# Kernel tuning notes

Hardware: AMD Instinct MI355X
Metric: run time of the kernel (lower is better)

Reference implementation:

```python
import jax, jax.numpy as jnp
import numpy as np

B, D_IN, C, P = 8192, 2048, 1000, 256


def setup_inputs() -> dict:
    key = jax.random.key(0)
    ks = jax.random.split(key, 6)
    return {
        "x": jax.random.normal(ks[0], (B, D_IN), dtype=jnp.float32),
        "Wm": jax.random.normal(ks[1], (C, D_IN), dtype=jnp.float32) * (1.0 / np.sqrt(D_IN)),
        "bm": jax.random.normal(ks[2], (C,), dtype=jnp.float32) * 0.01,
        "u": jax.random.normal(ks[3], (P, C), dtype=jnp.float32),
        "v": jax.random.normal(ks[4], (P, C), dtype=jnp.float32),
        "w": jax.random.normal(ks[5], (P, 1), dtype=jnp.float32),
    }


def reference(x, Wm, bm, u, v, w):
    # Backbone: Linear(D_IN -> C) producing per-instance logits (B, C)
    preds = jnp.einsum("bd,cd->bc", x, Wm) + bm
    # Gated attention, fully batched (replaces per-instance Python loop):
    # tanh(u @ pred) * sigmoid(v @ pred)  -> (B, P)
    gated = jnp.tanh(jnp.einsum("bc,pc->bp", preds, u)) * jax.nn.sigmoid(
        jnp.einsum("bc,pc->bp", preds, v)
    )
    scores = (gated @ w).ravel()          # (B,)
    attention = jax.nn.softmax(scores)    # softmax over instances
    total_pred = jnp.sum(preds * attention[:, None])
    return preds, total_pred
```

## Files before the change

kernel.cpp:

```cpp
#include <hip/hip_runtime.h>
#include <hip/hip_fp16.h>

typedef _Float16 half8 __attribute__((ext_vector_type(8)));
typedef float f32x4 __attribute__((ext_vector_type(4)));

#define B_   8192
#define DIN  2048
#define C_   1000
#define CP   1024
#define NP2  512

static const size_t OFF_WH  = 0;
static const size_t OFF_UVH = OFF_WH  + (size_t)CP * DIN * 2;
static const size_t OFF_PH  = OFF_UVH + (size_t)NP2 * CP * 2;
static const size_t OFF_SC  = OFF_PH  + (size_t)B_ * CP * 2;
static const size_t OFF_RS  = OFF_SC  + (size_t)B_ * 4;
static const size_t WS_NEED = OFF_RS  + (size_t)B_ * 4;

#define FENCE asm volatile("" ::: "memory")
#define BARRIER do { FENCE; __builtin_amdgcn_s_barrier(); FENCE; } while (0)
#define VMCNT(n) asm volatile("s_waitcnt vmcnt(" #n ")" ::: "memory")
#define PRIO1 __builtin_amdgcn_s_setprio(1)
#define PRIO0 __builtin_amdgcn_s_setprio(0)

__device__ __forceinline__ void gload16(const void* g, void* l) {
  __builtin_amdgcn_global_load_lds(
      (const __attribute__((address_space(1))) void*)g,
      (__attribute__((address_space(3))) void*)l, 16, 0, 0);
}

__global__ __launch_bounds__(256) void prep_kernel(
    const float* __restrict__ Wm,
    const float* __restrict__ u, const float* __restrict__ v,
    _Float16* __restrict__ wh, _Float16* __restrict__ uvh,
    float* __restrict__ scores, float* __restrict__ rowsum)
{
  const long NW  = (long)CP * DIN / 8;
  const long NUV = (long)NP2 * CP / 8;
  const long NZ  = 2 * (long)B_ / 8;
  const long T   = NW + NUV + NZ;
  for (long idx = (long)blockIdx.x * blockDim.x + threadIdx.x; idx < T;
       idx += (long)gridDim.x * blockDim.x) {
    if (idx < NW) {
      long e = idx * 8;
      int row = (int)(e >> 11);
      half8 h;
      if (row < C_) {
        float4 p0 = *(const float4*)(Wm + e);
        float4 p1 = *(const float4*)(Wm + e + 4);
        h[0] = (_Float16)p0.x; h[1] = (_Float16)p0.y; h[2] = (_Float16)p0.z; h[3] = (_Float16)p0.w;
        h[4] = (_Float16)p1.x; h[5] = (_Float16)p1.y; h[6] = (_Float16)p1.z; h[7] = (_Float16)p1.w;
      } else {
        h = (half8)(_Float16)0.f;
      }
      *(half8*)(wh + e) = h;
    } else if (idx < NW + NUV) {
      long e = (idx - NW) * 8;
      int j = (int)(e >> 10);
      int k = (int)(e & 1023);
      const float* src = (j & 1) ? v : u;
      int p = j >> 1;
      half8 h;
      #pragma unroll
      for (int t = 0; t < 8; ++t) {
        int kk = k + t;
        h[t] = (kk < C_) ? (_Float16)src[(size_t)p * C_ + kk] : (_Float16)0.f;
      }
      *(half8*)(uvh + e) = h;
    } else {
      long e = (idx - NW - NUV) * 8;
      float4 z = {0.f, 0.f, 0.f, 0.f};
      if (e < B_) {
        *(float4*)(scores + e) = z; *(float4*)(scores + e + 4) = z;
      } else {
        long r = e - B_;
        *(float4*)(rowsum + r) = z; *(float4*)(rowsum + r + 4) = z;
      }
    }
  }
}

__global__ __launch_bounds__(512, 2) void gemm1_kernel(
    const float* __restrict__ x, const _Float16* __restrict__ wh,
    const float* __restrict__ bmv, float* __restrict__ preds,
    _Float16* __restrict__ predsh, float* __restrict__ rowsum)
{
  __shared__ __align__(16) char LB[3 * 32768 + 3 * 8192];
  const int tid  = threadIdx.x;
  const int lane = tid & 63;
  const int w    = tid >> 6;
  const int wm   = w >> 1;
  const int wn   = w & 1;
  const int bm0  = blockIdx.x * 256;
  const int bn0  = blockIdx.y * 128;

  f32x4 acc[4][4] = {};

  const int trow = tid >> 3;
  const float* pAx = x + (size_t)(bm0 + trow) * DIN + (((tid & 7) ^ (trow & 7)) << 2);
  const int brow = tid >> 2;
  const _Float16* pBx = wh + (size_t)(bn0 + brow) * DIN + ((((tid & 3) ^ ((brow >> 1) & 3)) << 3));

  int aoff[4][2], boff[4];
  #pragma unroll
  for (int m = 0; m < 4; ++m) {
    int ra = wm * 64 + m * 16 + (lane & 15);
    int c0 = (lane >> 4) * 2;
    aoff[m][0] = ra * 128 + (((c0)     ^ (ra & 7)) << 4);
    aoff[m][1] = ra * 128 + (((c0 + 1) ^ (ra & 7)) << 4);
  }
  #pragma unroll
  for (int n = 0; n < 4; ++n) {
    int rb = wn * 64 + n * 16 + (lane & 15);
    boff[n] = rb * 64 + ((((lane >> 4)) ^ ((rb >> 1) & 3)) << 4);
  }

  half8 Aa[4], Ba[4], Ab[4], Bb[4];

  auto stage = [&](int c) {
    #pragma unroll
    for (int k = 0; k < 4; ++k)
      gload16(pAx + (size_t)k * 64 * DIN, LB + c * 32768 + k * 8192 + w * 1024);
    gload16(pBx, LB + 98304 + c * 8192 + w * 1024);
    pAx += 32; pBx += 32;
  };
  auto rdFrag = [&](int c, half8 (&A)[4], half8 (&Bf)[4]) {
    const char* ab = LB + c * 32768;
    const char* bb = LB + 98304 + c * 8192;
    #pragma unroll
    for (int m = 0; m < 4; ++m) {
      f32x4 lo = *(const f32x4*)(ab + aoff[m][0]);
      f32x4 hi = *(const f32x4*)(ab + aoff[m][1]);
      half8 h;
      h[0] = (_Float16)lo[0]; h[1] = (_Float16)lo[1];
      h[2] = (_Float16)lo[2]; h[3] = (_Float16)lo[3];
      h[4] = (_Float16)hi[0]; h[5] = (_Float16)hi[1];
      h[6] = (_Float16)hi[2]; h[7] = (_Float16)hi[3];
      A[m] = h;
    }
    #pragma unroll
    for (int n = 0; n < 4; ++n)
      Bf[n] = *(const half8*)(bb + boff[n]);
  };
  auto mfAll = [&](half8 (&A)[4], half8 (&Bf)[4]) {
    PRIO1;
    #pragma unroll
    for (int m = 0; m < 4; ++m)
      #pragma unroll
      for (int n = 0; n < 4; ++n)
        acc[m][n] = __builtin_amdgcn_mfma_f32_16x16x32_f16(A[m], Bf[n], acc[m][n], 0, 0, 0);
    PRIO0;
  };

  stage(0);
  stage(1);
  VMCNT(5);
  BARRIER;
  rdFrag(0, Aa, Ba);

  int c0 = 0;
  #pragma unroll 1
  for (int t = 0; t < 62; t += 2) {
    const int c1 = (c0 == 2) ? 0 : c0 + 1;
    const int c2 = (c1 == 2) ? 0 : c1 + 1;

    stage(c2);
    VMCNT(5);
    BARRIER;
    rdFrag(c1, Ab, Bb);
    mfAll(Aa, Ba);
    BARRIER;

    stage(c0);
    VMCNT(5);
    BARRIER;
    rdFrag(c2, Aa, Ba);
    mfAll(Ab, Bb);
    BARRIER;

    c0 = c2;
  }

  VMCNT(0);
  BARRIER;
  rdFrag(0, Ab, Bb);
  mfAll(Aa, Ba);
  mfAll(Ab, Bb);

  float rp[4][4] = {};
  #pragma unroll
  for (int m = 0; m < 4; ++m) {
    #pragma unroll
    for (int n = 0; n < 4; ++n) {
      f32x4 d = acc[m][n];
      int gc = bn0 + wn * 64 + n * 16 + (lane & 15);
      float bias = (gc < C_) ? bmv[gc] : 0.f;
      #pragma unroll
      for (int j = 0; j < 4; ++j) {
        int gr = bm0 + wm * 64 + m * 16 + (lane >> 4) * 4 + j;
        float val = d[j] + bias;
        predsh[(size_t)gr * CP + gc] = (_Float16)val;
        if (gc < C_) preds[(size_t)gr * C_ + gc] = val;
        rp[m][j] += val;
      }
    }
  }
  #pragma unroll
  for (int m = 0; m < 4; ++m) {
    #pragma unroll
    for (int j = 0; j < 4; ++j) {
      float s = rp[m][j];
      s += __shfl_xor(s, 1); s += __shfl_xor(s, 2);
      s += __shfl_xor(s, 4); s += __shfl_xor(s, 8);
      if ((lane & 15) == 0) {
        int gr = bm0 + wm * 64 + m * 16 + (lane >> 4) * 4 + j;
        atomicAdd(&rowsum[gr], s);
      }
    }
  }
}

__global__ __launch_bounds__(256) void gemm2_kernel(
    const _Float16* __restrict__ predsh, const _Float16* __restrict__ uvh,
    const float* __restrict__ wv, float* __restrict__ scores)
{
  __shared__ _Float16 sA[2][64 * 64];
  __shared__ _Float16 sB[2][128 * 64];
  const int tid  = threadIdx.x;
  const int lane = tid & 63;
  const int w    = tid >> 6;
  const int wm   = w >> 1, wn = w & 1;
  const int bm0  = blockIdx.x * 64;
  const int bn0  = blockIdx.y * 128;

  f32x4 acc[2][4] = {};

  const _Float16* srcA[2]; const _Float16* srcB[4];
  #pragma unroll
  for (int i = 0; i < 2; ++i) {
    int slot = i * 256 + tid;
    int row  = slot >> 3;
    int cb   = (slot & 7) << 4;
    int scb  = cb ^ ((row & 7) << 4);
    srcA[i] = predsh + (size_t)(bm0 + row) * CP + (scb >> 1);
  }
  #pragma unroll
  for (int i = 0; i < 4; ++i) {
    int slot = i * 256 + tid;
    int row  = slot >> 3;
    int cb   = (slot & 7) << 4;
    int scb  = cb ^ ((row & 7) << 4);
    srcB[i] = uvh + (size_t)(bn0 + row) * CP + (scb >> 1);
  }
  int aoff[2][2], boff[4][2];
  #pragma unroll
  for (int ks = 0; ks < 2; ++ks) {
    int kb = ks * 64 + (lane >> 4) * 16;
    #pragma unroll
    for (int mi = 0; mi < 2; ++mi) {
      int ra = wm * 32 + mi * 16 + (lane & 15);
      aoff[mi][ks] = ra * 128 + (kb ^ ((ra & 7) << 4));
    }
    #pragma unroll
    for (int ni = 0; ni < 4; ++ni) {
      int rb = wn * 64 + ni * 16 + (lane & 15);
      boff[ni][ks] = rb * 128 + (kb ^ ((rb & 7) << 4));
    }
  }

  auto stage = [&](int c) {
    #pragma unroll
    for (int i = 0; i < 2; ++i) {
      gload16(srcA[i], &sA[c][(i * 4 + w) * 512]);
      srcA[i] += 64;
    }
    #pragma unroll
    for (int i = 0; i < 4; ++i) {
      gload16(srcB[i], &sB[c][(i * 4 + w) * 512]);
      srcB[i] += 64;
    }
  };

  auto compute = [&](int c) {
    const char* bA = (const char*)&sA[c][0];
    const char* bB = (const char*)&sB[c][0];
    #pragma unroll
    for (int ks = 0; ks < 2; ++ks) {
      half8 a[2], b[4];
      #pragma unroll
      for (int mi = 0; mi < 2; ++mi) a[mi] = *(const half8*)(bA + aoff[mi][ks]);
      #pragma unroll
      for (int ni = 0; ni < 4; ++ni) b[ni] = *(const half8*)(bB + boff[ni][ks]);
      #pragma unroll
      for (int mi = 0; mi < 2; ++mi)
        #pragma unroll
        for (int ni = 0; ni < 4; ++ni)
          acc[mi][ni] = __builtin_amdgcn_mfma_f32_16x16x32_f16(a[mi], b[ni], acc[mi][ni], 0, 0, 0);
    }
  };

  const int NT = CP / 64;
  stage(0);
  #pragma unroll 1
  for (int kt = 0; kt < NT; kt += 2) {
    stage(1);
    asm volatile("s_waitcnt vmcnt(6)" ::: "memory");
    BARRIER;
    compute(0);
    BARRIER;
    if (kt + 2 < NT) {
      stage(0);
      asm volatile("s_waitcnt vmcnt(6)" ::: "memory");
    } else {
      asm volatile("s_waitcnt vmcnt(0)" ::: "memory");
    }
    BARRIER;
    compute(1);
    BARRIER;
  }

  float sp[2][4] = {};
  #pragma unroll
  for (int mi = 0; mi < 2; ++mi) {
    #pragma unroll
    for (int ni = 0; ni < 4; ++ni) {
      f32x4 d = acc[mi][ni];
      int gc = bn0 + wn * 64 + ni * 16 + (lane & 15);
      float wq = wv[gc >> 1];
      bool even = ((gc & 1) == 0);
      #pragma unroll
      for (int j = 0; j < 4; ++j) {
        float t  = d[j];
        float pr = __shfl_xor(t, 1);
        float th = 2.f / (1.f + __expf(-2.f * t)) - 1.f;
        float sg = 1.f / (1.f + __expf(-pr));
        sp[mi][j] += even ? (th * sg * wq) : 0.f;
      }
    }
  }
  #pragma unroll
  for (int mi = 0; mi < 2; ++mi) {
    #pragma unroll
    for (int j = 0; j < 4; ++j) {
      float s = sp[mi][j];
      s += __shfl_xor(s, 1); s += __shfl_xor(s, 2);
      s += __shfl_xor(s, 4); s += __shfl_xor(s, 8);
      if ((lane & 15) == 0) {
        int gr = bm0 + wm * 32 + mi * 16 + (lane >> 4) * 4 + j;
        atomicAdd(&scores[gr], s);
      }
    }
  }
}

__global__ __launch_bounds__(1024) void final_kernel(
    const float* __restrict__ scores, const float* __restrict__ rowsum,
    float* __restrict__ out)
{
  __shared__ float red[16], red2[16];
  const int t = threadIdx.x;
  const int lane = t & 63, wid = t >> 6;
  float s[8];
  float m = -3.4e38f;
  #pragma unroll
  for (int i = 0; i < 8; ++i) { s[i] = scores[t + i * 1024]; m = fmaxf(m, s[i]); }
  #pragma unroll
  for (int off = 1; off < 64; off <<= 1) m = fmaxf(m, __shfl_xor(m, off));
  if (lane == 0) red[wid] = m;
  __syncthreads();
  #pragma unroll
  for (int i = 0; i < 16; ++i) m = fmaxf(m, red[i]);
  __syncthreads();

  float se = 0.f, sr = 0.f;
  #pragma unroll
  for (int i = 0; i < 8; ++i) {
    float e = __expf(s[i] - m);
    se += e;
    sr += e * rowsum[t + i * 1024];
  }
  #pragma unroll
  for (int off = 1; off < 64; off <<= 1) { se += __shfl_xor(se, off); sr += __shfl_xor(sr, off); }
  if (lane == 0) { red[wid] = se; red2[wid] = sr; }
  __syncthreads();
  if (t == 0) {
    float tse = 0.f, tsr = 0.f;
    for (int i = 0; i < 16; ++i) { tse += red[i]; tsr += red2[i]; }
    out[0] = tsr / tse;
  }
}

extern "C" void kernel_launch(void* const* d_in, const int* in_sizes, int n_in,
                              void* d_out, int out_size, void* d_ws, size_t ws_size,
                              hipStream_t stream)
{
  const float* x   = (const float*)d_in[0];
  const float* Wm  = (const float*)d_in[1];
  const float* bmv = (const float*)d_in[2];
  const float* u   = (const float*)d_in[3];
  const float* v   = (const float*)d_in[4];
  const float* wv  = (const float*)d_in[5];
  float* out = (float*)d_out;

  if (ws_size < WS_NEED) return;

  char* ws = (char*)d_ws;
  _Float16* wh     = (_Float16*)(ws + OFF_WH);
  _Float16* uvh    = (_Float16*)(ws + OFF_UVH);
  _Float16* predsh = (_Float16*)(ws + OFF_PH);
  float*    scores = (float*)(ws + OFF_SC);
  float*    rowsum = (float*)(ws + OFF_RS);

  prep_kernel<<<1288, 256, 0, stream>>>(Wm, u, v, wh, uvh, scores, rowsum);
  gemm1_kernel<<<dim3(32, 8), 512, 0, stream>>>(x, wh, bmv, out, predsh, rowsum);
  gemm2_kernel<<<dim3(128, 4), 256, 0, stream>>>(predsh, uvh, wv, scores);
  final_kernel<<<1, 1024, 0, stream>>>(scores, rowsum, out + (size_t)B_ * C_);
}
```

Measured before the change: 93.59 us.

## Pre-convert x to fp16 and restructure gemm1 pipeline with 64-wide K tiles

```diff
diff --git a/kernel.cpp b/kernel.cpp
--- a/kernel.cpp
+++ b/kernel.cpp
@@ -10,7 +10,8 @@
 #define CP   1024
 #define NP2  512
 
-static const size_t OFF_WH  = 0;
+static const size_t OFF_XH  = 0;
+static const size_t OFF_WH  = OFF_XH  + (size_t)B_ * DIN * 2;
 static const size_t OFF_UVH = OFF_WH  + (size_t)CP * DIN * 2;
 static const size_t OFF_PH  = OFF_UVH + (size_t)NP2 * CP * 2;
 static const size_t OFF_SC  = OFF_PH  + (size_t)B_ * CP * 2;
@@ -20,6 +21,8 @@
 #define FENCE asm volatile("" ::: "memory")
 #define BARRIER do { FENCE; __builtin_amdgcn_s_barrier(); FENCE; } while (0)
 #define VMCNT(n) asm volatile("s_waitcnt vmcnt(" #n ")" ::: "memory")
+#define LGKM(n)  asm volatile("s_waitcnt lgkmcnt(" #n ")" ::: "memory")
+#define SCHED0   __builtin_amdgcn_sched_barrier(0)
 #define PRIO1 __builtin_amdgcn_s_setprio(1)
 #define PRIO0 __builtin_amdgcn_s_setprio(0)
 
@@ -30,19 +33,29 @@
 }
 
 __global__ __launch_bounds__(256) void prep_kernel(
-    const float* __restrict__ Wm,
+    const float* __restrict__ x, const float* __restrict__ Wm,
     const float* __restrict__ u, const float* __restrict__ v,
-    _Float16* __restrict__ wh, _Float16* __restrict__ uvh,
-    float* __restrict__ scores, float* __restrict__ rowsum)
+    _Float16* __restrict__ xh, _Float16* __restrict__ wh,
+    _Float16* __restrict__ uvh, float* __restrict__ scores,
+    float* __restrict__ rowsum)
 {
+  const long NX  = (long)B_ * DIN / 8;
   const long NW  = (long)CP * DIN / 8;
   const long NUV = (long)NP2 * CP / 8;
   const long NZ  = 2 * (long)B_ / 8;
-  const long T   = NW + NUV + NZ;
+  const long T   = NX + NW + NUV + NZ;
   for (long idx = (long)blockIdx.x * blockDim.x + threadIdx.x; idx < T;
        idx += (long)gridDim.x * blockDim.x) {
-    if (idx < NW) {
+    if (idx < NX) {
       long e = idx * 8;
+      float4 p0 = *(const float4*)(x + e);
+      float4 p1 = *(const float4*)(x + e + 4);
+      half8 h;
+      h[0] = (_Float16)p0.x; h[1] = (_Float16)p0.y; h[2] = (_Float16)p0.z; h[3] = (_Float16)p0.w;
+      h[4] = (_Float16)p1.x; h[5] = (_Float16)p1.y; h[6] = (_Float16)p1.z; h[7] = (_Float16)p1.w;
+      *(half8*)(xh + e) = h;
+    } else if (idx < NX + NW) {
+      long e = (idx - NX) * 8;
       int row = (int)(e >> 11);
       half8 h;
       if (row < C_) {
@@ -54,8 +67,8 @@
         h = (half8)(_Float16)0.f;
       }
       *(half8*)(wh + e) = h;
-    } else if (idx < NW + NUV) {
-      long e = (idx - NW) * 8;
+    } else if (idx < NX + NW + NUV) {
+      long e = (idx - NX - NW) * 8;
       int j = (int)(e >> 10);
       int k = (int)(e & 1023);
       const float* src = (j & 1) ? v : u;
@@ -68,7 +81,7 @@
       }
       *(half8*)(uvh + e) = h;
     } else {
-      long e = (idx - NW - NUV) * 8;
+      long e = (idx - NX - NW - NUV) * 8;
       float4 z = {0.f, 0.f, 0.f, 0.f};
       if (e < B_) {
         *(float4*)(scores + e) = z; *(float4*)(scores + e + 4) = z;
@@ -80,12 +93,13 @@
   }
 }
 
-__global__ __launch_bounds__(512, 2) void gemm1_kernel(
-    const float* __restrict__ x, const _Float16* __restrict__ wh,
+__global__ __launch_bounds__(512, 1) void gemm1_kernel(
+    const _Float16* __restrict__ xh, const _Float16* __restrict__ wh,
     const float* __restrict__ bmv, float* __restrict__ preds,
     _Float16* __restrict__ predsh, float* __restrict__ rowsum)
 {
-  __shared__ __align__(16) char LB[3 * 32768 + 3 * 8192];
+  __shared__ _Float16 lds[(3 * 32768 + 3 * 16384) / 2];
+  char* const LB = (char*)lds;
   const int tid  = threadIdx.x;
   const int lane = tid & 63;
   const int w    = tid >> 6;
@@ -97,95 +111,122 @@
   f32x4 acc[4][4] = {};
 
   const int trow = tid >> 3;
-  const float* pAx = x + (size_t)(bm0 + trow) * DIN + (((tid & 7) ^ (trow & 7)) << 2);
-  const int brow = tid >> 2;
-  const _Float16* pBx = wh + (size_t)(bn0 + brow) * DIN + ((((tid & 3) ^ ((brow >> 1) & 3)) << 3));
-
-  int aoff[4][2], boff[4];
-  #pragma unroll
-  for (int m = 0; m < 4; ++m) {
-    int ra = wm * 64 + m * 16 + (lane & 15);
-    int c0 = (lane >> 4) * 2;
-    aoff[m][0] = ra * 128 + (((c0)     ^ (ra & 7)) << 4);
-    aoff[m][1] = ra * 128 + (((c0 + 1) ^ (ra & 7)) << 4);
-  }
-  #pragma unroll
-  for (int n = 0; n < 4; ++n) {
-    int rb = wn * 64 + n * 16 + (lane & 15);
-    boff[n] = rb * 64 + ((((lane >> 4)) ^ ((rb >> 1) & 3)) << 4);
-  }
-
-  half8 Aa[4], Ba[4], Ab[4], Bb[4];
-
-  auto stage = [&](int c) {
-    #pragma unroll
-    for (int k = 0; k < 4; ++k)
-      gload16(pAx + (size_t)k * 64 * DIN, LB + c * 32768 + k * 8192 + w * 1024);
-    gload16(pBx, LB + 98304 + c * 8192 + w * 1024);
-    pAx += 32; pBx += 32;
-  };
-  auto rdFrag = [&](int c, half8 (&A)[4], half8 (&Bf)[4]) {
-    const char* ab = LB + c * 32768;
-    const char* bb = LB + 98304 + c * 8192;
-    #pragma unroll
-    for (int m = 0; m < 4; ++m) {
-      f32x4 lo = *(const f32x4*)(ab + aoff[m][0]);
-      f32x4 hi = *(const f32x4*)(ab + aoff[m][1]);
-      half8 h;
-      h[0] = (_Float16)lo[0]; h[1] = (_Float16)lo[1];
-      h[2] = (_Float16)lo[2]; h[3] = (_Float16)lo[3];
-      h[4] = (_Float16)hi[0]; h[5] = (_Float16)hi[1];
-      h[6] = (_Float16)hi[2]; h[7] = (_Float16)hi[3];
-      A[m] = h;
-    }
-    #pragma unroll
-    for (int n = 0; n < 4; ++n)
-      Bf[n] = *(const half8*)(bb + boff[n]);
-  };
-  auto mfAll = [&](half8 (&A)[4], half8 (&Bf)[4]) {
+  const int swzc = (((tid & 7) << 4) ^ ((trow & 7) << 4)) >> 1;
+  const _Float16* pA = xh + (size_t)(bm0 + trow) * DIN + swzc;
+  const _Float16* pB = wh + (size_t)(bn0 + trow) * DIN + swzc;
+
+  int aoff[4][2], boff[4][2];
+  #pragma unroll
+  for (int m = 0; m < 4; ++m)
+    #pragma unroll
+    for (int ks = 0; ks < 2; ++ks) {
+      int ra = wm * 64 + m * 16 + (lane & 15);
+      int kb = ks * 64 + (lane >> 4) * 16;
+      aoff[m][ks] = ra * 128 + (kb ^ ((ra & 7) << 4));
+    }
+  #pragma unroll
+  for (int n = 0; n < 4; ++n)
+    #pragma unroll
+    for (int ks = 0; ks < 2; ++ks) {
+      int rb = wn * 64 + n * 16 + (lane & 15);
+      int kb = ks * 64 + (lane >> 4) * 16;
+      boff[n][ks] = rb * 128 + (kb ^ ((rb & 7) << 4));
+    }
+
+  half8 A[4][2], Bf[4][2];
+
+  auto stageH1 = [&](int c) {
+    #pragma unroll
+    for (int k = 0; k < 3; ++k)
+      gload16(pA + (size_t)k * 64 * DIN, LB + c * 32768 + k * 8192 + w * 1024);
+  };
+  auto stageH2 = [&](int c) {
+    gload16(pA + (size_t)3 * 64 * DIN, LB + c * 32768 + 3 * 8192 + w * 1024);
+    #pragma unroll
+    for (int k = 0; k < 2; ++k)
+      gload16(pB + (size_t)k * 64 * DIN, LB + 98304 + c * 16384 + k * 8192 + w * 1024);
+    pA += 64; pB += 64;
+  };
+  auto rdA = [&](int c) {
+    const char* b = LB + c * 32768;
+    #pragma unroll
+    for (int m = 0; m < 4; ++m)
+      #pragma unroll
+      for (int ks = 0; ks < 2; ++ks)
+        A[m][ks] = *(const half8*)(b + aoff[m][ks]);
+  };
+  auto rdB01 = [&](int c) {
+    const char* b = LB + 98304 + c * 16384;
+    #pragma unroll
+    for (int n = 0; n < 2; ++n)
+      #pragma unroll
+      for (int ks = 0; ks < 2; ++ks)
+        Bf[n][ks] = *(const half8*)(b + boff[n][ks]);
+  };
+  auto rdB23 = [&](int c) {
+    const char* b = LB + 98304 + c * 16384;
+    #pragma unroll
+    for (int n = 2; n < 4; ++n)
+      #pragma unroll
+      for (int ks = 0; ks < 2; ++ks)
+        Bf[n][ks] = *(const half8*)(b + boff[n][ks]);
+  };
+  auto mfH = [&](int nlo) {
     PRIO1;
     #pragma unroll
     for (int m = 0; m < 4; ++m)
       #pragma unroll
-      for (int n = 0; n < 4; ++n)
-        acc[m][n] = __builtin_amdgcn_mfma_f32_16x16x32_f16(A[m], Bf[n], acc[m][n], 0, 0, 0);
+      for (int n = nlo; n < nlo + 2; ++n)
+        #pragma unroll
+        for (int ks = 0; ks < 2; ++ks)
+          acc[m][n] = __builtin_amdgcn_mfma_f32_16x16x32_f16(A[m][ks], Bf[n][ks], acc[m][n], 0, 0, 0);
     PRIO0;
   };
 
-  stage(0);
-  stage(1);
-  VMCNT(5);
+  stageH1(0); stageH2(0);
+  stageH1(1); stageH2(1);
+  VMCNT(6);
   BARRIER;
-  rdFrag(0, Aa, Ba);
 
   int c0 = 0;
   #pragma unroll 1
-  for (int t = 0; t < 62; t += 2) {
-    const int c1 = (c0 == 2) ? 0 : c0 + 1;
-    const int c2 = (c1 == 2) ? 0 : c1 + 1;
-
-    stage(c2);
-    VMCNT(5);
-    BARRIER;
-    rdFrag(c1, Ab, Bb);
-    mfAll(Aa, Ba);
-    BARRIER;
-
-    stage(c0);
-    VMCNT(5);
-    BARRIER;
-    rdFrag(c2, Aa, Ba);
-    mfAll(Ab, Bb);
-    BARRIER;
-
-    c0 = c2;
-  }
-
+  for (int t = 0; t < 30; ++t) {
+    const int c2 = (c0 >= 1) ? c0 - 1 : 2;
+
+    rdA(c0); rdB01(c0);
+    stageH1(c2);
+    LGKM(8);
+    BARRIER;
+    LGKM(0); SCHED0;
+    mfH(0);
+    BARRIER;
+
+    rdB23(c0);
+    stageH2(c2);
+    VMCNT(6);
+    BARRIER;
+    LGKM(0); SCHED0;
+    mfH(2);
+    BARRIER;
+
+    c0 = (c0 == 2) ? 0 : c0 + 1;
+  }
+
+  rdA(0); rdB01(0);
+  BARRIER;
+  LGKM(0); SCHED0;
+  mfH(0);
+  BARRIER;
+  rdB23(0);
   VMCNT(0);
   BARRIER;
-  rdFrag(0, Ab, Bb);
-  mfAll(Aa, Ba);
-  mfAll(Ab, Bb);
+  LGKM(0); SCHED0;
+  mfH(2);
+  BARRIER;
+  rdA(1); rdB01(1);
+  mfH(0);
+  rdB23(1);
+  mfH(2);
 
   float rp[4][4] = {};
   #pragma unroll
@@ -405,14 +446,15 @@
   if (ws_size < WS_NEED) return;
 
   char* ws = (char*)d_ws;
+  _Float16* xh     = (_Float16*)(ws + OFF_XH);
   _Float16* wh     = (_Float16*)(ws + OFF_WH);
   _Float16* uvh    = (_Float16*)(ws + OFF_UVH);
   _Float16* predsh = (_Float16*)(ws + OFF_PH);
   float*    scores = (float*)(ws + OFF_SC);
   float*    rowsum = (float*)(ws + OFF_RS);
 
-  prep_kernel<<<1288, 256, 0, stream>>>(Wm, u, v, wh, uvh, scores, rowsum);
-  gemm1_kernel<<<dim3(32, 8), 512, 0, stream>>>(x, wh, bmv, out, predsh, rowsum);
+  prep_kernel<<<2048, 256, 0, stream>>>(x, Wm, u, v, xh, wh, uvh, scores, rowsum);
+  gemm1_kernel<<<dim3(32, 8), 512, 0, stream>>>(xh, wh, bmv, out, predsh, rowsum);
   gemm2_kernel<<<dim3(128, 4), 256, 0, stream>>>(predsh, uvh, wv, scores);
   final_kernel<<<1, 1024, 0, stream>>>(scores, rowsum, out + (size_t)B_ * C_);
 }
```

New measurement: 92.05 us. No clear change (-1.6%).
